# Kernel optimization log

Hardware: AMD Instinct MI355X
Metric: run time of the kernel (lower is better)

The kernel has to match this reference:

```python
import jax, jax.numpy as jnp
import numpy as np

N_WORDS = 4096
N_HEADS = 512
EMB = 768          # input_size
HID = 1024         # hidden_size
DIST = 64          # dist_emb_size (forced by Conv1d(64, ...))
SENT_LEN = 64      # fixed sentence length -> static max padded length
PAIR_F = 2 * EMB + DIST  # 1600


def setup_inputs() -> dict:
    key = jax.random.key(0)
    ks = jax.random.split(key, 14)
    words = jax.random.normal(ks[0], (N_WORDS, EMB), dtype=jnp.float32)
    heads_ids = jax.random.randint(ks[1], (N_HEADS,), 0, N_WORDS, dtype=jnp.int64)
    sent_id = (jnp.arange(N_WORDS) // SENT_LEN).astype(jnp.int32)  # sorted, contiguous sentences
    s = 0.02
    return {
        "words": words,
        "heads_ids": heads_ids,
        "sent_id": sent_id,
        "emb_table": jax.random.normal(ks[2], (128, DIST), dtype=jnp.float32) * s,
        "W1": jax.random.normal(ks[3], (PAIR_F, HID), dtype=jnp.float32) * s,
        "b1": jnp.zeros((HID,), jnp.float32),
        "W2": jax.random.normal(ks[4], (HID, 256), dtype=jnp.float32) * s,
        "b2": jnp.zeros((256,), jnp.float32),
        "W3": jax.random.normal(ks[5], (256, DIST), dtype=jnp.float32) * s,
        "b3": jnp.zeros((DIST,), jnp.float32),
        "cw1": jax.random.normal(ks[6], (4, DIST, 3), dtype=jnp.float32) * s,  # Conv1d(64,4,3,1,1)
        "cb1": jnp.zeros((4,), jnp.float32),
        "cw2": jax.random.normal(ks[7], (2, 4, 3), dtype=jnp.float32) * s,    # Conv1d(4,2,3,1,1)
        "cb2": jnp.zeros((2,), jnp.float32),
    }


def _conv1d(x, w, b):
    # x: [N, C_in, L], w: [C_out, C_in, 3], padding=1, stride=1 (torch Conv1d semantics)
    y = jax.lax.conv_general_dilated(x, w, window_strides=(1,), padding=((1, 1),),
                                     dimension_numbers=("NCH", "OIH", "NCH"))
    return y + b[None, :, None]


def reference(words, heads_ids, sent_id, emb_table, W1, b1, W2, b2, W3, b3, cw1, cb1, cw2, cb2):
    n_words = words.shape[0]
    heads = heads_ids.astype(jnp.int32)
    H = heads.shape[0]

    # relative positions & distance-embedding ids, clamped to bucket 127 outside [-63, 63]
    rel = heads[:, None] - jnp.arange(n_words, dtype=jnp.int32)[None, :]      # [H, W]
    eid = rel + 63
    eid = jnp.where((eid < 0) | (eid > 126), 127, eid)

    # per-head sentence span (sent_id is sorted & contiguous)
    sh = sent_id[heads]
    starts = jnp.searchsorted(sent_id, sh, side="left")
    lengths = jnp.searchsorted(sent_id, sh, side="right") - starts            # [H]

    # padded ragged layout: row i holds words of head i's sentence, left-packed
    j = jnp.arange(SENT_LEN, dtype=jnp.int32)
    cols = starts[:, None] + j[None, :]                                       # [H, L]
    mask = j[None, :] < lengths[:, None]                                      # [H, L]
    cols_c = jnp.clip(cols, 0, n_words - 1)

    head_w = words[heads]                                                     # [H, E]
    col_w = words[cols_c]                                                     # [H, L, E]
    dist = emb_table[jnp.take_along_axis(eid, cols_c, axis=1)]                # [H, L, DIST]
    feat = jnp.concatenate(
        [jnp.broadcast_to(head_w[:, None, :], col_w.shape), col_w, dist], axis=-1)
    feat = jnp.where(mask[..., None], feat, jnp.zeros((), feat.dtype))        # zero padding rows (as torch)

    # FFNN (dropout is identity in eval mode)
    x = jax.nn.relu(feat @ W1 + b1)
    x = jax.nn.relu(x @ W2 + b2)
    x = x @ W3 + b3                                                           # [H, L, 64]

    # conv stack over the padded ragged axis
    x = _conv1d(x.transpose(0, 2, 1), cw1, cb1)
    x = _conv1d(x, cw2, cb2)
    res = x.transpose(0, 2, 1)                                                # [H, L, 2]

    # scatter back into [H, n_words, 2]; masked slots get out-of-range col -> dropped
    rows = jnp.broadcast_to(jnp.arange(H, dtype=jnp.int32)[:, None], mask.shape)
    cols_sc = jnp.where(mask, cols, n_words)
    scores = jnp.full((H, n_words, 2), -jnp.inf, dtype=words.dtype)
    scores = scores.at[rows, cols_sc].set(res, mode="drop")

    # eval-mode validity log-mask
    valid_starts = jnp.log((rel >= 0).astype(words.dtype))
    valid_ends = jnp.log((rel <= 0).astype(words.dtype))
    valid = jnp.stack([valid_starts, valid_ends], axis=2)
    return scores + valid
```

## Files before the change

### kernel.cpp

```cpp
#include <hip/hip_runtime.h>
#include <math.h>

#define NW   4096
#define NH   512
#define EMBD 768
#define HIDD 1024
#define DISTD 64
#define SLEN 64

#define NEG_BIG (-1.0e30f)

typedef __attribute__((ext_vector_type(8))) short short8;
typedef __attribute__((ext_vector_type(16))) float f32x16;
typedef __attribute__((ext_vector_type(4))) float f32x4;

#define MFMA32(a, b, c) __builtin_amdgcn_mfma_f32_32x32x16_bf16((a), (b), (c), 0, 0, 0)
#define MFMA16(a, b, c) __builtin_amdgcn_mfma_f32_16x16x32_bf16((a), (b), (c), 0, 0, 0)

__device__ __forceinline__ unsigned short f2bf(float f) {
    unsigned u = __float_as_uint(f);
    u += 0x7FFFu + ((u >> 16) & 1u);
    return (unsigned short)(u >> 16);
}
__device__ __forceinline__ float bf2f(unsigned short s) {
    return __uint_as_float(((unsigned)s) << 16);
}
__device__ __forceinline__ unsigned cvtpk(float lo, float hi) {
    unsigned r;
    asm("v_cvt_pk_bf16_f32 %0, %1, %2" : "=v"(r) : "v"(lo), "v"(hi));
    return r;
}
__device__ __forceinline__ short8 pack8(float f0, float f1, float f2, float f3,
                                        float f4, float f5, float f6, float f7) {
    union { unsigned u[4]; short8 s; } r;
    r.u[0] = cvtpk(f0, f1); r.u[1] = cvtpk(f2, f3);
    r.u[2] = cvtpk(f4, f5); r.u[3] = cvtpk(f6, f7);
    return r.s;
}

__device__ __forceinline__ void pack_b32_dev(long t, const float* __restrict__ src,
                                             int ld, int nb32, int KB,
                                             unsigned short* __restrict__ dst)
{
    int l = (int)(t & 63); long u = t >> 6;
    int nb = (int)(u % nb32); int kb = (int)(u / nb32);
    int row0 = kb * 16 + ((l >> 5) << 3);
    int col  = (nb << 5) + (l & 31);
    const float* s = src + (size_t)row0 * ld + col;
    short8 v;
#pragma unroll
    for (int j = 0; j < 8; ++j) v[j] = (short)f2bf(s[(size_t)j * ld]);
    *(short8*)(dst + (((size_t)nb * KB + kb) << 9) + l * 8) = v;
}

__device__ __forceinline__ void pack_b16_dev(long t, const float* __restrict__ src,
                                             int ld, int nb16, int KB,
                                             unsigned short* __restrict__ dst)
{
    int l = (int)(t & 63); long u = t >> 6;
    int nb = (int)(u % nb16); int kb = (int)(u / nb16);
    int row0 = kb * 32 + ((l >> 4) << 3);
    int col  = (nb << 4) + (l & 15);
    const float* s = src + (size_t)row0 * ld + col;
    short8 v;
#pragma unroll
    for (int j = 0; j < 8; ++j) v[j] = (short)f2bf(s[(size_t)j * ld]);
    *(short8*)(dst + (((size_t)nb * KB + kb) << 9) + l * 8) = v;
}

__device__ __forceinline__ void cvt8_dev(long i, const float* __restrict__ src,
                                         unsigned short* __restrict__ dst)
{
    const float* s = src + i * 8;
    short8 v;
#pragma unroll
    for (int j = 0; j < 8; ++j) v[j] = (short)f2bf(s[j]);
    *(short8*)(dst + i * 8) = v;
}

__global__ __launch_bounds__(256)
void prep_kernel(const float* __restrict__ words, const float* __restrict__ emb,
                 const float* __restrict__ W1, const float* __restrict__ W2,
                 const float* __restrict__ W3,
                 const int* __restrict__ heads, const int* __restrict__ sent_id,
                 unsigned short* __restrict__ wordsb, unsigned short* __restrict__ wpack,
                 unsigned short* __restrict__ embb,
                 unsigned short* __restrict__ W1pa, unsigned short* __restrict__ W1px,
                 unsigned short* __restrict__ W1pd,
                 unsigned short* __restrict__ W2p, unsigned short* __restrict__ W3p,
                 int* __restrict__ starts, int* __restrict__ lens)
{
    const int b = blockIdx.x, tid = threadIdx.x;
    if (b < 1536) {
        cvt8_dev((long)b * 256 + tid, words, wordsb);
    } else if (b < 3072) {
        long t = (long)(b - 1536) * 256 + tid;
        int r = (int)(t / 96), g = (int)(t % 96);
        const float* s = words + (size_t)r * EMBD + g * 8;
        short8 v;
#pragma unroll
        for (int j = 0; j < 8; ++j) v[j] = (short)f2bf(s[j]);
        int m = r >> 5, kb = g >> 1, lane = (r & 31) + 32 * (g & 1);
        *(short8*)(wpack + (((size_t)m * 48 + kb) << 9) + lane * 8) = v;
    } else if (b < 3076) {
        cvt8_dev((long)(b - 3072) * 256 + tid, emb, embb);
    } else if (b < 3460) {
        pack_b32_dev((long)(b - 3076) * 256 + tid, W1, HIDD, 32, 48, W1pa);
    } else if (b < 3844) {
        pack_b32_dev((long)(b - 3460) * 256 + tid, W1 + (size_t)768 * HIDD, HIDD, 32, 48, W1px);
    } else if (b < 3876) {
        pack_b32_dev((long)(b - 3844) * 256 + tid, W1 + (size_t)1536 * HIDD, HIDD, 32, 4, W1pd);
    } else if (b < 4004) {
        pack_b32_dev((long)(b - 3876) * 256 + tid, W2, 256, 8, 64, W2p);
    } else if (b < 4012) {
        pack_b16_dev((long)(b - 4004) * 256 + tid, W3, 64, 4, 8, W3p);
    } else {
        int h = (b - 4012) * 256 + tid;
        if (h < NH) {
            int head = heads[h];
            int s = sent_id[head];
            int lo = 0, hi = NW;
            while (lo < hi) { int mid = (lo + hi) >> 1; if (sent_id[mid] < s) lo = mid + 1; else hi = mid; }
            int start = lo;
            lo = 0; hi = NW;
            while (lo < hi) { int mid = (lo + hi) >> 1; if (sent_id[mid] <= s) lo = mid + 1; else hi = mid; }
            int len = lo - start;
            if (len > SLEN) len = SLEN;
            starts[h] = start;
            lens[h] = len;
        }
    }
}

__global__ __launch_bounds__(256, 4)
void gemms_kernel(const unsigned short* __restrict__ wordsb,
                  const unsigned short* __restrict__ wpack,
                  const unsigned short* __restrict__ embb,
                  const unsigned short* __restrict__ W1pa,
                  const unsigned short* __restrict__ W1px,
                  const unsigned short* __restrict__ W1pd,
                  const float* __restrict__ b1, const int* __restrict__ heads,
                  unsigned short* __restrict__ XwP, unsigned short* __restrict__ Hcb,
                  unsigned short* __restrict__ Dtb)
{
    const int b = blockIdx.x, tid = threadIdx.x;
    const int l = tid & 63, w = tid >> 6;

    if (b < 1024) {
        const int mB = b >> 3, nB = b & 7;
        const int cbg = nB * 4 + w;
        const unsigned short* ap = wpack + (((size_t)mB * 48) << 9) + l * 8;
        const unsigned short* bp = W1px + (((size_t)cbg * 48) << 9) + l * 8;
        f32x16 acc = {};
#pragma unroll
        for (int kk = 0; kk < 48; ++kk) {
            short8 a = *(const short8*)(ap + ((size_t)kk << 9));
            short8 bb = *(const short8*)(bp + ((size_t)kk << 9));
            acc = MFMA32(a, bb, acc);
        }
        const int col = cbg * 32 + (l & 31);
        const float bv = b1[col];
        const int kb2 = 2 * cbg + ((l & 31) >> 4);
        const int j = l & 7;
        const int lhalf = 32 * ((l >> 3) & 1);
        unsigned short* cp = XwP + (((size_t)mB * 64 + kb2) << 9) + j;
#pragma unroll
        for (int r = 0; r < 16; ++r) {
            int rr = (r & 3) + 8 * (r >> 2) + 4 * (l >> 5);
            cp[(rr + lhalf) * 8] = f2bf(acc[r] + bv);
        }
    } else if (b < 1152) {
        const int q = b - 1024;
        const int mB = q >> 3, nB = q & 7;
        const int cbg = nB * 4 + w;
        int row = heads[mB * 32 + (l & 31)];
        const unsigned short* ap = wordsb + (size_t)row * EMBD + ((l >> 5) << 3);
        const unsigned short* bp = W1pa + (((size_t)cbg * 48) << 9) + l * 8;
        f32x16 acc = {};
#pragma unroll
        for (int kk = 0; kk < 48; ++kk) {
            short8 a = *(const short8*)(ap + kk * 16);
            short8 bb = *(const short8*)(bp + ((size_t)kk << 9));
            acc = MFMA32(a, bb, acc);
        }
        const int col = cbg * 32 + (l & 31);
#pragma unroll
        for (int r = 0; r < 16; ++r) {
            int rr = mB * 32 + (r & 3) + 8 * (r >> 2) + 4 * (l >> 5);
            Hcb[(size_t)rr * HIDD + col] = f2bf(acc[r]);
        }
    } else {
        const int q = b - 1152;
        const int mB = q >> 3, nB = q & 7;
        const int cbg = nB * 4 + w;
        const unsigned short* ap = embb + (size_t)(mB * 32 + (l & 31)) * DISTD + ((l >> 5) << 3);
        const unsigned short* bp = W1pd + (((size_t)cbg * 4) << 9) + l * 8;
        f32x16 acc = {};
#pragma unroll
        for (int kk = 0; kk < 4; ++kk) {
            short8 a = *(const short8*)(ap + kk * 16);
            short8 bb = *(const short8*)(bp + ((size_t)kk << 9));
            acc = MFMA32(a, bb, acc);
        }
        const int col = cbg * 32 + (l & 31);
#pragma unroll
        for (int r = 0; r < 16; ++r) {
            int rr = mB * 32 + (r & 3) + 8 * (r >> 2) + 4 * (l >> 5);
            Dtb[(size_t)rr * HIDD + col] = f2bf(acc[r]);
        }
    }
}

__global__ __launch_bounds__(256)
void packd_kernel(const unsigned short* __restrict__ Dtb,
                  unsigned short* __restrict__ PDr)
{
    const int tid = threadIdx.x, l = tid & 63;
    const int c = blockIdx.x * 4 + (tid >> 6);
    const int s = c / 192, rem = c % 192;
    const int m = rem >> 6, kb = rem & 63;
    const int row = 126 - (s + 32 * m + (l & 31));
    const int koff = kb * 16 + ((l >> 5) << 3);
    short8 v = *(const short8*)(Dtb + (size_t)row * HIDD + koff);
    *(short8*)(PDr + ((size_t)c << 9) + l * 8) = v;
}

#define NT 32
__global__ __launch_bounds__(512)
void head_kernel(const unsigned short* __restrict__ XwP,
                 const unsigned short* __restrict__ Hcb,
                 const unsigned short* __restrict__ PDr,
                 const unsigned short* __restrict__ W2p,
                 const float* __restrict__ b2,
                 const unsigned short* __restrict__ W3p,
                 const float* __restrict__ b3,
                 const float* __restrict__ cw1, const float* __restrict__ cb1,
                 const float* __restrict__ cw2, const float* __restrict__ cb2,
                 const int* __restrict__ heads, const int* __restrict__ starts,
                 const int* __restrict__ lens,
                 float* __restrict__ out)
{
    __shared__ char smem[67584];
    unsigned short* Ast = (unsigned short*)smem;
    unsigned short* Bst = (unsigned short*)(smem + 16384);
    unsigned short* x2s = (unsigned short*)smem;
    float* x3s = (float*)smem;
    float* y1s = (float*)(smem + 35328);
    float* y2s = (float*)(smem + 37376);

    const int tid = threadIdx.x;
    const int l = tid & 63, w = tid >> 6;
    const int h0 = blockIdx.x * 2;

    const int head0 = heads[h0],  head1 = heads[h0 + 1];
    const int strt0 = starts[h0], strt1 = starts[h0 + 1];
    const int len0  = lens[h0],   len1  = lens[h0 + 1];

    const int kkA = w >> 2, rb = w & 3;
    const int hbA = rb >> 1;
    const int headA = hbA ? head1 : head0;
    const int strtA = hbA ? strt1 : strt0;
    const int q0A = 63 - (headA - strtA);
    const unsigned short* xwPp =
        XwP + (((size_t)((strtA >> 5) + (rb & 1)) * 64) << 9) + l * 8;
    const unsigned short* ddPp =
        PDr + (((size_t)((q0A & 31) * 3 + (q0A >> 5) + (rb & 1)) * 64) << 9) + l * 8;
    const unsigned short* hcp = Hcb + (size_t)(h0 + hbA) * HIDD + ((l >> 5) << 3);
    const int kkB = w >> 2, nbB0 = (w & 3) * 2;
    const int mb = w & 1, nq = w >> 1;

    f32x16 acc[2][2] = {};

    short8 rxw, rhc, rdd, rb0, rb1;

#define LOADT(t)                                                              \
    {                                                                         \
        const int kb_ = (t) * 2 + kkA;                                        \
        rxw = *(const short8*)(xwPp + ((size_t)kb_ << 9));                    \
        rdd = *(const short8*)(ddPp + ((size_t)kb_ << 9));                    \
        rhc = *(const short8*)(hcp + kb_ * 16);                               \
        const size_t c0_ = ((size_t)(nbB0 * 64 + (t) * 2 + kkB)) << 9;        \
        rb0 = *(const short8*)(W2p + c0_ + l * 8);                            \
        rb1 = *(const short8*)(W2p + c0_ + 32768 + l * 8);                    \
    }

#define WRITET(t)                                                             \
    {                                                                         \
        const int buf_ = (t) & 1;                                             \
        float f_[8];                                                          \
        _Pragma("unroll")                                                     \
        for (int j = 0; j < 8; ++j)                                           \
            f_[j] = fmaxf(bf2f((unsigned short)rxw[j])                        \
                        + bf2f((unsigned short)rhc[j])                        \
                        + bf2f((unsigned short)rdd[j]), 0.f);                 \
        short8 v_ = pack8(f_[0], f_[1], f_[2], f_[3], f_[4], f_[5], f_[6], f_[7]); \
        *(short8*)&Ast[buf_ * 4096 + (kkA * 4 + rb) * 512 + l * 8] = v_;      \
        *(short8*)&Bst[buf_ * 8192 + (kkB * 8 + nbB0) * 512 + l * 8] = rb0;   \
        *(short8*)&Bst[buf_ * 8192 + (kkB * 8 + nbB0 + 1) * 512 + l * 8] = rb1; \
    }

    LOADT(0);
    WRITET(0);
    LOADT(1);
    __syncthreads();

#pragma unroll 2
    for (int t = 0; t < NT; ++t) {
        const int buf = t & 1;
        short8 af0[2], af1[2], bf0[2], bf1[2];
#pragma unroll
        for (int k2 = 0; k2 < 2; ++k2) {
            af0[k2] = *(const short8*)&Ast[buf * 4096 + (k2 * 4 + mb * 2 + 0) * 512 + l * 8];
            af1[k2] = *(const short8*)&Ast[buf * 4096 + (k2 * 4 + mb * 2 + 1) * 512 + l * 8];
            bf0[k2] = *(const short8*)&Bst[buf * 8192 + (k2 * 8 + nq * 2 + 0) * 512 + l * 8];
            bf1[k2] = *(const short8*)&Bst[buf * 8192 + (k2 * 8 + nq * 2 + 1) * 512 + l * 8];
        }
        if (t + 1 < NT) WRITET(t + 1);
        if (t + 2 < NT) LOADT(t + 2);
        __builtin_amdgcn_s_setprio(1);
#pragma unroll
        for (int k2 = 0; k2 < 2; ++k2) {
            acc[0][0] = MFMA32(af0[k2], bf0[k2], acc[0][0]);
            acc[0][1] = MFMA32(af0[k2], bf1[k2], acc[0][1]);
            acc[1][0] = MFMA32(af1[k2], bf0[k2], acc[1][0]);
            acc[1][1] = MFMA32(af1[k2], bf1[k2], acc[1][1]);
        }
        __builtin_amdgcn_s_setprio(0);
        __syncthreads();
    }

#pragma unroll
    for (int i = 0; i < 2; ++i) {
#pragma unroll
        for (int n = 0; n < 2; ++n) {
            const int ct = nq * 64 + n * 32 + (l & 31);
            const float bv = b2[ct];
#pragma unroll
            for (int r = 0; r < 16; ++r) {
                const int rt = mb * 64 + i * 32 + (r & 3) + 8 * (r >> 2) + 4 * (l >> 5);
                const int hb = rt >> 6, rl = rt & 63;
                x2s[hb * 16896 + rl * 264 + ct] = f2bf(fmaxf(acc[i][n][r] + bv, 0.f));
            }
        }
    }
    __syncthreads();

    {
        const int hb = w >> 2, q = w & 3;
        const unsigned short* x2h = x2s + hb * 16896;
        f32x4 acc2[4] = {};
#pragma unroll
        for (int kk = 0; kk < 8; ++kk) {
            short8 bf = *(const short8*)(W3p + ((q * 8 + kk) << 9) + l * 8);
#pragma unroll
            for (int mi = 0; mi < 4; ++mi) {
                short8 af = *(const short8*)&x2h[(mi * 16 + (l & 15)) * 264 + kk * 32 + ((l >> 4) << 3)];
                acc2[mi] = MFMA16(af, bf, acc2[mi]);
            }
        }
        __syncthreads();
        float* x3h = x3s + hb * 4416;
        const int col = q * 16 + (l & 15);
        const float b3v = b3[col];
#pragma unroll
        for (int mi = 0; mi < 4; ++mi) {
#pragma unroll
            for (int r = 0; r < 4; ++r) {
                const int rowv = mi * 16 + (l >> 4) * 4 + r;
                x3h[rowv * 69 + col] = acc2[mi][r] + b3v;
            }
        }
    }
    __syncthreads();

    {
        const int hb3 = tid >> 8;
        const int co = (tid >> 6) & 3;
        const int ll = tid & 63;
        const float* x3h = x3s + hb3 * 4416;
        float s = cb1[co];
        const float* wb = cw1 + co * DISTD * 3;
        for (int ci = 0; ci < DISTD; ++ci) {
            float w0 = wb[ci * 3 + 0], w1 = wb[ci * 3 + 1], w2v = wb[ci * 3 + 2];
            float xm = (ll > 0) ? x3h[(ll - 1) * 69 + ci] : 0.f;
            float xc = x3h[ll * 69 + ci];
            float xp = (ll < 63) ? x3h[(ll + 1) * 69 + ci] : 0.f;
            s = fmaf(xm, w0, s);
            s = fmaf(xc, w1, s);
            s = fmaf(xp, w2v, s);
        }
        y1s[hb3 * 256 + co * 64 + ll] = s;
    }
    __syncthreads();

    if (tid < 256) {
        const int hb4 = tid >> 7;
        const int co = (tid >> 6) & 1;
        const int ll = tid & 63;
        const float* yh = y1s + hb4 * 256;
        const int head = hb4 ? head1 : head0;
        const int strt = hb4 ? strt1 : strt0;
        float s = cb2[co];
#pragma unroll
        for (int ci = 0; ci < 4; ++ci) {
            const float* wb = cw2 + (co * 4 + ci) * 3;
            const float* yr = yh + ci * 64;
            float xm = (ll > 0) ? yr[ll - 1] : 0.f;
            float xc = yr[ll];
            float xp = (ll < 63) ? yr[ll + 1] : 0.f;
            s = fmaf(xm, wb[0], s);
            s = fmaf(xc, wb[1], s);
            s = fmaf(xp, wb[2], s);
        }
        const int col = strt + ll;
        const int rel = head - col;
        const bool valid = (co == 0) ? (rel >= 0) : (rel <= 0);
        y2s[hb4 * 128 + ll * 2 + co] = valid ? s : NEG_BIG;
    }
    __syncthreads();

    {
        const int hb = tid >> 8;
        const int c8 = tid & 255;
        const int strt = hb ? strt1 : strt0;
        const int len  = hb ? len1  : len0;
        float* orow = out + ((size_t)(h0 + hb) * NW) * 2;
        const float* yh = y2s + hb * 128;
#pragma unroll
        for (int i = 0; i < 16; ++i) {
            const int col = i * 256 + c8;
            float2 v;
            if (col >= strt && col < strt + len) {
                v = *(const float2*)&yh[(col - strt) * 2];
            } else {
                v.x = NEG_BIG; v.y = NEG_BIG;
            }
            *(float2*)&orow[(size_t)col * 2] = v;
        }
    }
}

extern "C" void kernel_launch(void* const* d_in, const int* in_sizes, int n_in,
                              void* d_out, int out_size, void* d_ws, size_t ws_size,
                              hipStream_t stream)
{
    const float* words = (const float*)d_in[0];
    const int* heads   = (const int*)d_in[1];
    const int* sent_id = (const int*)d_in[2];
    const float* emb   = (const float*)d_in[3];
    const float* W1    = (const float*)d_in[4];
    const float* b1    = (const float*)d_in[5];
    const float* W2    = (const float*)d_in[6];
    const float* b2    = (const float*)d_in[7];
    const float* W3    = (const float*)d_in[8];
    const float* b3    = (const float*)d_in[9];
    const float* cw1   = (const float*)d_in[10];
    const float* cb1   = (const float*)d_in[11];
    const float* cw2   = (const float*)d_in[12];
    const float* cb2   = (const float*)d_in[13];
    float* out = (float*)d_out;

    char* wsb = (char*)d_ws;
    unsigned short* XwP  = (unsigned short*)(wsb + 0);
    unsigned short* Hcb  = (unsigned short*)(wsb + 8388608);
    unsigned short* Dtb  = (unsigned short*)(wsb + 9437184);
    unsigned short* W2p  = (unsigned short*)(wsb + 9699328);
    unsigned short* W3p  = (unsigned short*)(wsb + 10223616);
    unsigned short* PDr  = (unsigned short*)(wsb + 10256384);
    unsigned short* embb = (unsigned short*)(wsb + 16547840);
    int* starts          = (int*)(wsb + 16564224);
    int* lens            = (int*)(wsb + 16566272);
    char* ob = (char*)d_out;
    unsigned short* wordsb = (unsigned short*)(ob + 0);
    unsigned short* wpack  = (unsigned short*)(ob + 6291456);
    unsigned short* W1pa   = (unsigned short*)(ob + 12582912);
    unsigned short* W1px   = (unsigned short*)(ob + 14155776);
    unsigned short* W1pd   = (unsigned short*)(ob + 15728640);
    (void)ws_size; (void)in_sizes; (void)n_in; (void)out_size;

    prep_kernel<<<dim3(4014), dim3(256), 0, stream>>>(
        words, emb, W1, W2, W3, heads, sent_id,
        wordsb, wpack, embb, W1pa, W1px, W1pd, W2p, W3p, starts, lens);

    gemms_kernel<<<dim3(1184), dim3(256), 0, stream>>>(
        wordsb, wpack, embb, W1pa, W1px, W1pd, b1, heads, XwP, Hcb, Dtb);

    packd_kernel<<<dim3(1536), dim3(256), 0, stream>>>(Dtb, PDr);

    head_kernel<<<dim3(NH / 2), dim3(512), 0, stream>>>(
        XwP, Hcb, PDr, W2p, b2, W3p, b3, cw1, cb1, cw2, cb2,
        heads, starts, lens, out);
}
```

Baseline: 76.14 us.

## Drop duplicate bf16 words copy, pack via LDS, stage GEMM output stores

```diff
diff --git a/kernel.cpp b/kernel.cpp
--- a/kernel.cpp
+++ b/kernel.cpp
@@ -78,44 +78,53 @@
     *(short8*)(dst + i * 8) = v;
 }
 
+#define WPS 776
 __global__ __launch_bounds__(256)
 void prep_kernel(const float* __restrict__ words, const float* __restrict__ emb,
                  const float* __restrict__ W1, const float* __restrict__ W2,
                  const float* __restrict__ W3,
                  const int* __restrict__ heads, const int* __restrict__ sent_id,
-                 unsigned short* __restrict__ wordsb, unsigned short* __restrict__ wpack,
-                 unsigned short* __restrict__ embb,
+                 unsigned short* __restrict__ wpack, unsigned short* __restrict__ embb,
                  unsigned short* __restrict__ W1pa, unsigned short* __restrict__ W1px,
                  unsigned short* __restrict__ W1pd,
                  unsigned short* __restrict__ W2p, unsigned short* __restrict__ W3p,
                  int* __restrict__ starts, int* __restrict__ lens)
 {
+    __shared__ unsigned short tls[32 * WPS];
+
     const int b = blockIdx.x, tid = threadIdx.x;
-    if (b < 1536) {
-        cvt8_dev((long)b * 256 + tid, words, wordsb);
-    } else if (b < 3072) {
-        long t = (long)(b - 1536) * 256 + tid;
-        int r = (int)(t / 96), g = (int)(t % 96);
-        const float* s = words + (size_t)r * EMBD + g * 8;
-        short8 v;
-#pragma unroll
-        for (int j = 0; j < 8; ++j) v[j] = (short)f2bf(s[j]);
-        int m = r >> 5, kb = g >> 1, lane = (r & 31) + 32 * (g & 1);
-        *(short8*)(wpack + (((size_t)m * 48 + kb) << 9) + lane * 8) = v;
-    } else if (b < 3076) {
-        cvt8_dev((long)(b - 3072) * 256 + tid, emb, embb);
-    } else if (b < 3460) {
-        pack_b32_dev((long)(b - 3076) * 256 + tid, W1, HIDD, 32, 48, W1pa);
-    } else if (b < 3844) {
-        pack_b32_dev((long)(b - 3460) * 256 + tid, W1 + (size_t)768 * HIDD, HIDD, 32, 48, W1px);
-    } else if (b < 3876) {
-        pack_b32_dev((long)(b - 3844) * 256 + tid, W1 + (size_t)1536 * HIDD, HIDD, 32, 4, W1pd);
-    } else if (b < 4004) {
-        pack_b32_dev((long)(b - 3876) * 256 + tid, W2, 256, 8, 64, W2p);
-    } else if (b < 4012) {
-        pack_b16_dev((long)(b - 4004) * 256 + tid, W3, 64, 4, 8, W3p);
+    if (b < 128) {
+        const int m = b;
+#pragma unroll
+        for (int i = 0; i < 24; ++i) {
+            const int idx = tid + i * 256;
+            const int r = idx / 192, c4 = (idx % 192) * 4;
+            float4 v = *(const float4*)(words + ((size_t)(m * 32 + r)) * EMBD + c4);
+            tls[r * WPS + c4 + 0] = f2bf(v.x);
+            tls[r * WPS + c4 + 1] = f2bf(v.y);
+            tls[r * WPS + c4 + 2] = f2bf(v.z);
+            tls[r * WPS + c4 + 3] = f2bf(v.w);
+        }
+        __syncthreads();
+        const int l = tid & 63, w = tid >> 6;
+        for (int kb = w; kb < 48; kb += 4) {
+            short8 v = *(const short8*)&tls[(l & 31) * WPS + kb * 16 + ((l >> 5) << 3)];
+            *(short8*)(wpack + (((size_t)m * 48 + kb) << 9) + l * 8) = v;
+        }
+    } else if (b < 132) {
+        cvt8_dev((long)(b - 128) * 256 + tid, emb, embb);
+    } else if (b < 516) {
+        pack_b32_dev((long)(b - 132) * 256 + tid, W1, HIDD, 32, 48, W1pa);
+    } else if (b < 900) {
+        pack_b32_dev((long)(b - 516) * 256 + tid, W1 + (size_t)768 * HIDD, HIDD, 32, 48, W1px);
+    } else if (b < 932) {
+        pack_b32_dev((long)(b - 900) * 256 + tid, W1 + (size_t)1536 * HIDD, HIDD, 32, 4, W1pd);
+    } else if (b < 1060) {
+        pack_b32_dev((long)(b - 932) * 256 + tid, W2, 256, 8, 64, W2p);
+    } else if (b < 1068) {
+        pack_b16_dev((long)(b - 1060) * 256 + tid, W3, 64, 4, 8, W3p);
     } else {
-        int h = (b - 4012) * 256 + tid;
+        int h = (b - 1068) * 256 + tid;
         if (h < NH) {
             int head = heads[h];
             int s = sent_id[head];
@@ -133,8 +142,7 @@
 }
 
 __global__ __launch_bounds__(256, 4)
-void gemms_kernel(const unsigned short* __restrict__ wordsb,
-                  const unsigned short* __restrict__ wpack,
+void gemms_kernel(const unsigned short* __restrict__ wpack,
                   const unsigned short* __restrict__ embb,
                   const unsigned short* __restrict__ W1pa,
                   const unsigned short* __restrict__ W1px,
@@ -143,6 +151,8 @@
                   unsigned short* __restrict__ XwP, unsigned short* __restrict__ Hcb,
                   unsigned short* __restrict__ Dtb)
 {
+    __shared__ unsigned short tls[4][32 * 40];
+
     const int b = blockIdx.x, tid = threadIdx.x;
     const int l = tid & 63, w = tid >> 6;
 
@@ -160,26 +170,28 @@
         }
         const int col = cbg * 32 + (l & 31);
         const float bv = b1[col];
-        const int kb2 = 2 * cbg + ((l & 31) >> 4);
-        const int j = l & 7;
-        const int lhalf = 32 * ((l >> 3) & 1);
-        unsigned short* cp = XwP + (((size_t)mB * 64 + kb2) << 9) + j;
+        unsigned short* tw = tls[w];
 #pragma unroll
         for (int r = 0; r < 16; ++r) {
-            int rr = (r & 3) + 8 * (r >> 2) + 4 * (l >> 5);
-            cp[(rr + lhalf) * 8] = f2bf(acc[r] + bv);
-        }
+            int rowl = (r & 3) + 8 * (r >> 2) + 4 * (l >> 5);
+            tw[rowl * 40 + (l & 31)] = f2bf(acc[r] + bv);
+        }
+        short8 v0 = *(const short8*)&tw[(l & 31) * 40 + ((l >> 5) << 3)];
+        short8 v1 = *(const short8*)&tw[(l & 31) * 40 + 16 + ((l >> 5) << 3)];
+        *(short8*)(XwP + (((size_t)(mB * 64 + cbg * 2)) << 9) + l * 8) = v0;
+        *(short8*)(XwP + (((size_t)(mB * 64 + cbg * 2 + 1)) << 9) + l * 8) = v1;
     } else if (b < 1152) {
         const int q = b - 1024;
         const int mB = q >> 3, nB = q & 7;
         const int cbg = nB * 4 + w;
         int row = heads[mB * 32 + (l & 31)];
-        const unsigned short* ap = wordsb + (size_t)row * EMBD + ((l >> 5) << 3);
+        const unsigned short* ap = wpack + (((size_t)(row >> 5) * 48) << 9)
+                                 + ((row & 31) + 32 * (l >> 5)) * 8;
         const unsigned short* bp = W1pa + (((size_t)cbg * 48) << 9) + l * 8;
         f32x16 acc = {};
 #pragma unroll
         for (int kk = 0; kk < 48; ++kk) {
-            short8 a = *(const short8*)(ap + kk * 16);
+            short8 a = *(const short8*)(ap + ((size_t)kk << 9));
             short8 bb = *(const short8*)(bp + ((size_t)kk << 9));
             acc = MFMA32(a, bb, acc);
         }
@@ -471,19 +483,18 @@
     int* starts          = (int*)(wsb + 16564224);
     int* lens            = (int*)(wsb + 16566272);
     char* ob = (char*)d_out;
-    unsigned short* wordsb = (unsigned short*)(ob + 0);
-    unsigned short* wpack  = (unsigned short*)(ob + 6291456);
-    unsigned short* W1pa   = (unsigned short*)(ob + 12582912);
-    unsigned short* W1px   = (unsigned short*)(ob + 14155776);
-    unsigned short* W1pd   = (unsigned short*)(ob + 15728640);
+    unsigned short* wpack  = (unsigned short*)(ob + 0);
+    unsigned short* W1pa   = (unsigned short*)(ob + 6291456);
+    unsigned short* W1px   = (unsigned short*)(ob + 7864320);
+    unsigned short* W1pd   = (unsigned short*)(ob + 9437184);
     (void)ws_size; (void)in_sizes; (void)n_in; (void)out_size;
 
-    prep_kernel<<<dim3(4014), dim3(256), 0, stream>>>(
+    prep_kernel<<<dim3(1070), dim3(256), 0, stream>>>(
         words, emb, W1, W2, W3, heads, sent_id,
-        wordsb, wpack, embb, W1pa, W1px, W1pd, W2p, W3p, starts, lens);
+        wpack, embb, W1pa, W1px, W1pd, W2p, W3p, starts, lens);
 
     gemms_kernel<<<dim3(1184), dim3(256), 0, stream>>>(
-        wordsb, wpack, embb, W1pa, W1px, W1pd, b1, heads, XwP, Hcb, Dtb);
+        wpack, embb, W1pa, W1px, W1pd, b1, heads, XwP, Hcb, Dtb);
 
     packd_kernel<<<dim3(1536), dim3(256), 0, stream>>>(Dtb, PDr);
 
```

New measurement: 77.22 us. About the same (+1.4%).
